# Performance work log

Measured on AMD Instinct MI355X. Metric: run time of the kernel, lower is better.

## Reference

```python
import jax, jax.numpy as jnp
import numpy as np

N_NODES = 50000
N_EDGES = 600000
N_FEAT = 128
N_DIMS = 128
N_CLSS = 10


def setup_inputs() -> dict:
    key = jax.random.key(0)
    ks = jax.random.split(key, 9)
    x = jax.random.normal(ks[0], (N_NODES, N_FEAT), dtype=jnp.float32)
    edge_index = jax.random.randint(ks[1], (2, N_EDGES), 0, N_NODES, dtype=jnp.int32)
    edge_weight = jax.random.uniform(ks[2], (N_EDGES,), dtype=jnp.float32)
    # Glorot-ish init for learned params
    W1 = jax.random.normal(ks[3], (N_FEAT, N_DIMS), dtype=jnp.float32) * (1.0 / np.sqrt(N_FEAT))
    b1 = jnp.zeros((N_DIMS,), dtype=jnp.float32)
    W2 = jax.random.normal(ks[4], (N_DIMS, N_DIMS), dtype=jnp.float32) * (1.0 / np.sqrt(N_DIMS))
    b2 = jnp.zeros((N_DIMS,), dtype=jnp.float32)
    Wc = jax.random.normal(ks[5], (N_DIMS, N_CLSS), dtype=jnp.float32) * (1.0 / np.sqrt(N_DIMS))
    bc = jnp.zeros((N_CLSS,), dtype=jnp.float32)
    return {"x": x, "edge_index": edge_index, "edge_weight": edge_weight,
            "W1": W1, "b1": b1, "W2": W2, "b2": b2, "Wc": Wc, "bc": bc}


def gcn_conv(x, W, b, src, dst, ew, n_nodes):
    """PyG GCNConv (add_self_loops=True, improved=False, bias=True).
    out[i] = sum_{(j->i) in E} d_i^-1/2 * w_ji * d_j^-1/2 * (xW)[j]
             + d_i^-1 * (xW)[i]  (self loop, weight 1) + b
    where d_i = 1 + sum of incoming edge weights at i.
    """
    h = x @ W                                                   # [N, D]
    deg = jax.ops.segment_sum(ew, dst, num_segments=n_nodes) + 1.0  # self-loop weight 1
    dinv = jax.lax.rsqrt(deg)                                   # deg >= 1, no inf
    norm = dinv[src] * ew * dinv[dst]                           # [E]
    agg = jax.ops.segment_sum(h[src] * norm[:, None], dst, num_segments=n_nodes)
    agg = agg + h * (dinv * dinv)[:, None]                      # self-loop term
    return agg + b


def reference(x, edge_index, edge_weight, W1, b1, W2, b2, Wc, bc):
    n = x.shape[0]
    src, dst = edge_index[0], edge_index[1]
    h = jax.nn.relu(gcn_conv(x, W1, b1, src, dst, edge_weight, n))
    # dropout is identity in eval mode
    h = gcn_conv(h, W2, b2, src, dst, edge_weight, n)
    h = jax.nn.relu(h)
    return h @ Wc + bc
```

## Files before the change

### kernel.cpp

```cpp
#include <hip/hip_runtime.h>
#include <hip/hip_bf16.h>

#define N_NODES 50000
#define N_EDGES 600000
#define NC 10

typedef __attribute__((ext_vector_type(8))) __bf16 bf16x8;
typedef __attribute__((ext_vector_type(4))) float f32x4;

__device__ __forceinline__ unsigned short f2bf(float f) {
    unsigned u = __float_as_uint(f);
    u += 0x7fff + ((u >> 16) & 1);
    return (unsigned short)(u >> 16);
}

__global__ void k_zero(int4* __restrict__ p, int n4) {
    int i = blockIdx.x * blockDim.x + threadIdx.x;
    if (i < n4) p[i] = make_int4(0, 0, 0, 0);
}

__global__ void k_x2b(const float4* __restrict__ in, ushort4* __restrict__ out, int n4) {
    int i = blockIdx.x * blockDim.x + threadIdx.x;
    if (i >= n4) return;
    float4 v = in[i];
    ushort4 o;
    o.x = f2bf(v.x); o.y = f2bf(v.y); o.z = f2bf(v.z); o.w = f2bf(v.w);
    out[i] = o;
}

__global__ void k_wt(const float* __restrict__ W, unsigned short* __restrict__ Wt) {
    int i = blockIdx.x * 256 + threadIdx.x;
    int n = i >> 7, k = i & 127;
    Wt[n * 128 + k] = f2bf(W[k * 128 + n]);
}

__global__ void k_count(const int4* __restrict__ dst4, int* __restrict__ cnt,
                        int4* __restrict__ ord4) {
    int i = blockIdx.x * blockDim.x + threadIdx.x;
    if (i >= N_EDGES / 4) return;
    int4 d = dst4[i];
    int4 o;
    o.x = atomicAdd(&cnt[d.x], 1);
    o.y = atomicAdd(&cnt[d.y], 1);
    o.z = atomicAdd(&cnt[d.z], 1);
    o.w = atomicAdd(&cnt[d.w], 1);
    ord4[i] = o;
}

__global__ void k_scan1(const int* __restrict__ cnt, int* __restrict__ rowptr,
                        int* __restrict__ bsum, int n) {
    __shared__ int sh[256];
    int t = threadIdx.x;
    int i = blockIdx.x * 256 + t;
    int v = (i < n) ? cnt[i] : 0;
    sh[t] = v;
    __syncthreads();
    for (int off = 1; off < 256; off <<= 1) {
        int x = 0;
        if (t >= off) x = sh[t - off];
        __syncthreads();
        sh[t] += x;
        __syncthreads();
    }
    if (i < n) rowptr[i] = sh[t] - v;
    if (t == 255) bsum[blockIdx.x] = sh[255];
}

__global__ void k_scan2(int* __restrict__ bsum, int nb) {
    __shared__ int sh[256];
    int t = threadIdx.x;
    int v = (t < nb) ? bsum[t] : 0;
    sh[t] = v;
    __syncthreads();
    for (int off = 1; off < 256; off <<= 1) {
        int x = 0;
        if (t >= off) x = sh[t - off];
        __syncthreads();
        sh[t] += x;
        __syncthreads();
    }
    if (t < nb) bsum[t] = sh[t] - v;
}

__global__ void k_scan3(int* __restrict__ rowptr, const int* __restrict__ bsum, int n) {
    int t = threadIdx.x;
    int i = blockIdx.x * 256 + t;
    if (i < n) rowptr[i] += bsum[blockIdx.x];
    if (blockIdx.x == 0 && t == 0) rowptr[n] = N_EDGES;
}

__global__ void k_scatter(const int* __restrict__ src, const int* __restrict__ dst,
                          const float* __restrict__ ew, const int* __restrict__ ord,
                          const int* __restrict__ rowptr,
                          int* __restrict__ esrc, float* __restrict__ ew2) {
    int e = blockIdx.x * blockDim.x + threadIdx.x;
    if (e >= N_EDGES) return;
    int pos = rowptr[dst[e]] + ord[e];
    esrc[pos] = src[e];
    ew2[pos]  = ew[e];
}

__global__ void k_deg(const int* __restrict__ rowptr, const float* __restrict__ ew2,
                      float* __restrict__ dinv) {
    int i = blockIdx.x * blockDim.x + threadIdx.x;
    if (i >= N_NODES) return;
    int p1 = rowptr[i + 1];
    float s = 1.0f;
    for (int p = rowptr[i]; p < p1; ++p) s += ew2[p];
    dinv[i] = rsqrtf(s);
}

__global__ void k_norm(const int* __restrict__ rowptr, const int* __restrict__ esrc,
                       const float* __restrict__ ew2, const float* __restrict__ dinv,
                       float* __restrict__ enorm) {
    int i = blockIdx.x * blockDim.x + threadIdx.x;
    if (i >= N_NODES) return;
    float di = dinv[i];
    int p  = rowptr[i];
    int p1 = rowptr[i + 1];
    for (; p + 4 <= p1; p += 4) {
        int s0 = esrc[p], s1 = esrc[p+1], s2 = esrc[p+2], s3 = esrc[p+3];
        float d0 = dinv[s0], d1 = dinv[s1], d2 = dinv[s2], d3 = dinv[s3];
        enorm[p]   = d0 * ew2[p]   * di;
        enorm[p+1] = d1 * ew2[p+1] * di;
        enorm[p+2] = d2 * ew2[p+2] * di;
        enorm[p+3] = d3 * ew2[p+3] * di;
    }
    for (; p < p1; ++p) enorm[p] = dinv[esrc[p]] * ew2[p] * di;
}

__global__ __launch_bounds__(256) void k_gemm_mfma(const unsigned short* __restrict__ Xb,
                                                   const unsigned short* __restrict__ Wt,
                                                   unsigned short* __restrict__ Yb, int M) {
    __shared__ unsigned short Al[64 * 128];
    __shared__ unsigned short Bl[128 * 128];
    int t = threadIdx.x;
    int row0 = blockIdx.x * 64;

    for (int i = t; i < 2048; i += 256) {
        int r = i >> 4, q = i & 15;
        *(bf16x8*)(Bl + r * 128 + ((q ^ (r & 7)) << 3)) =
            *(const bf16x8*)(Wt + r * 128 + (q << 3));
    }
    for (int i = t; i < 1024; i += 256) {
        int r = i >> 4, q = i & 15;
        int gr = row0 + r;
        bf16x8 v;
        if (gr < M) {
            v = *(const bf16x8*)(Xb + (size_t)gr * 128 + (q << 3));
        } else {
#pragma unroll
            for (int j = 0; j < 8; ++j) v[j] = (__bf16)0.0f;
        }
        *(bf16x8*)(Al + r * 128 + ((q ^ (r & 7)) << 3)) = v;
    }
    __syncthreads();

    int l  = t & 63;
    int w  = t >> 6;
    int ar = (w << 4) + (l & 15);
    int kq = l >> 4;

    bf16x8 af[4];
#pragma unroll
    for (int s = 0; s < 4; ++s) {
        int g = ((s << 2) + kq) ^ (l & 7);
        af[s] = *(const bf16x8*)(Al + ar * 128 + (g << 3));
    }

    f32x4 acc[8];
#pragma unroll
    for (int c = 0; c < 8; ++c)
#pragma unroll
        for (int j = 0; j < 4; ++j) acc[c][j] = 0.0f;

#pragma unroll
    for (int c = 0; c < 8; ++c) {
        int br = (c << 4) + (l & 15);
#pragma unroll
        for (int s = 0; s < 4; ++s) {
            int g = ((s << 2) + kq) ^ (l & 7);
            bf16x8 bf = *(const bf16x8*)(Bl + br * 128 + (g << 3));
            acc[c] = __builtin_amdgcn_mfma_f32_16x16x32_bf16(af[s], bf, acc[c], 0, 0, 0);
        }
    }

    int orow = row0 + (w << 4) + ((l >> 4) << 2);
    int ocol = l & 15;
#pragma unroll
    for (int c = 0; c < 8; ++c) {
#pragma unroll
        for (int j = 0; j < 4; ++j) {
            int r = orow + j;
            if (r < M) Yb[(size_t)r * 128 + (c << 4) + ocol] = f2bf(acc[c][j]);
        }
    }
}

template <int MODE>
__global__ __launch_bounds__(256) void k_agg(const unsigned* __restrict__ hb,
                                             const int* __restrict__ rowptr,
                                             const int* __restrict__ esrc,
                                             const float* __restrict__ enorm,
                                             const float* __restrict__ dinv,
                                             const float* __restrict__ bias,
                                             const float* __restrict__ Wc,
                                             const float* __restrict__ bc,
                                             float* __restrict__ out) {
    int wid  = (blockIdx.x * blockDim.x + threadIdx.x) >> 6;
    int lane = threadIdx.x & 63;
    if (wid >= N_NODES) return;
    wid = __builtin_amdgcn_readfirstlane(wid);
    int p  = __builtin_amdgcn_readfirstlane(rowptr[wid]);
    int p1 = __builtin_amdgcn_readfirstlane(rowptr[wid + 1]);
    float di  = dinv[wid];
    float di2 = di * di;
    unsigned sv = hb[(size_t)wid * 64 + lane];
    float2 acc;
    acc.x = __uint_as_float(sv << 16) * di2;
    acc.y = __uint_as_float(sv & 0xffff0000u) * di2;

    while (p + 12 <= p1) {
        int s[12]; float w[12]; unsigned v[12];
#pragma unroll
        for (int i = 0; i < 12; ++i) {
            s[i] = __builtin_amdgcn_readfirstlane(esrc[p + i]);
            w[i] = enorm[p + i];
        }
#pragma unroll
        for (int i = 0; i < 12; ++i) v[i] = hb[(size_t)s[i] * 64 + lane];
#pragma unroll
        for (int i = 0; i < 12; ++i) {
            acc.x += w[i] * __uint_as_float(v[i] << 16);
            acc.y += w[i] * __uint_as_float(v[i] & 0xffff0000u);
        }
        p += 12;
    }
    while (p + 4 <= p1) {
        int s[4]; float w[4]; unsigned v[4];
#pragma unroll
        for (int i = 0; i < 4; ++i) {
            s[i] = __builtin_amdgcn_readfirstlane(esrc[p + i]);
            w[i] = enorm[p + i];
        }
#pragma unroll
        for (int i = 0; i < 4; ++i) v[i] = hb[(size_t)s[i] * 64 + lane];
#pragma unroll
        for (int i = 0; i < 4; ++i) {
            acc.x += w[i] * __uint_as_float(v[i] << 16);
            acc.y += w[i] * __uint_as_float(v[i] & 0xffff0000u);
        }
        p += 4;
    }
    for (; p < p1; ++p) {
        int s = __builtin_amdgcn_readfirstlane(esrc[p]);
        float w = enorm[p];
        unsigned v = hb[(size_t)s * 64 + lane];
        acc.x += w * __uint_as_float(v << 16);
        acc.y += w * __uint_as_float(v & 0xffff0000u);
    }

    float2 bv = ((const float2*)bias)[lane];
    acc.x = fmaxf(acc.x + bv.x, 0.f);
    acc.y = fmaxf(acc.y + bv.y, 0.f);
    if (MODE == 0) {
        unsigned lo = f2bf(acc.x), hi = f2bf(acc.y);
        ((unsigned*)out)[(size_t)wid * 64 + lane] = lo | (hi << 16);
    } else {
        int k0 = 2 * lane;
        float r[NC];
#pragma unroll
        for (int c = 0; c < NC; ++c)
            r[c] = acc.x * Wc[k0 * NC + c] + acc.y * Wc[(k0 + 1) * NC + c];
#pragma unroll
        for (int off = 32; off; off >>= 1)
#pragma unroll
            for (int c = 0; c < NC; ++c)
                r[c] += __shfl_xor(r[c], off, 64);
        if (lane < NC) out[(size_t)wid * NC + lane] = r[lane] + bc[lane];
    }
}

extern "C" void kernel_launch(void* const* d_in, const int* in_sizes, int n_in,
                              void* d_out, int out_size, void* d_ws, size_t ws_size,
                              hipStream_t stream) {
    const float* x   = (const float*)d_in[0];
    const int*   ei  = (const int*)d_in[1];
    const float* ew  = (const float*)d_in[2];
    const float* W1  = (const float*)d_in[3];
    const float* b1  = (const float*)d_in[4];
    const float* W2  = (const float*)d_in[5];
    const float* b2  = (const float*)d_in[6];
    const float* Wc  = (const float*)d_in[7];
    const float* bc  = (const float*)d_in[8];
    float*       out = (float*)d_out;

    const int* src = ei;
    const int* dst = ei + N_EDGES;

    size_t off = 0;
    auto carve = [&](size_t bytes) {
        void* p = (char*)d_ws + off;
        off += (bytes + 255) & ~(size_t)255;
        return p;
    };
    unsigned short* xb  = (unsigned short*)carve((size_t)N_NODES * 128 * 2);
    unsigned short* hb  = (unsigned short*)carve((size_t)N_NODES * 128 * 2);
    unsigned short* hb1 = (unsigned short*)carve((size_t)N_NODES * 128 * 2);
    unsigned short* wt1 = (unsigned short*)carve(128 * 128 * 2);
    unsigned short* wt2 = (unsigned short*)carve(128 * 128 * 2);
    float* dinv   = (float*)carve((size_t)N_NODES * 4);
    int*   cnt    = (int*)carve((size_t)N_NODES * 4);
    int*   rowptr = (int*)carve((size_t)(N_NODES + 1) * 4);
    int*   bsum   = (int*)carve(256 * 4);
    int*   ord    = (int*)carve((size_t)N_EDGES * 4);
    int*   esrc   = (int*)carve((size_t)N_EDGES * 4);
    float* ew2    = (float*)carve((size_t)N_EDGES * 4);
    float* enorm  = (float*)carve((size_t)N_EDGES * 4);
    (void)ws_size; (void)n_in; (void)in_sizes; (void)out_size;

    int eb = (N_EDGES + 255) / 256;
    int nb = (N_NODES + 255) / 256;

    k_zero<<<(N_NODES / 4 + 255) / 256, 256, 0, stream>>>((int4*)cnt, N_NODES / 4);
    k_count<<<(N_EDGES / 4 + 255) / 256, 256, 0, stream>>>((const int4*)dst, cnt, (int4*)ord);
    k_scan1<<<nb, 256, 0, stream>>>(cnt, rowptr, bsum, N_NODES);
    k_scan2<<<1, 256, 0, stream>>>(bsum, nb);
    k_scan3<<<nb, 256, 0, stream>>>(rowptr, bsum, N_NODES);
    k_scatter<<<eb, 256, 0, stream>>>(src, dst, ew, ord, rowptr, esrc, ew2);
    k_deg<<<nb, 256, 0, stream>>>(rowptr, ew2, dinv);
    k_norm<<<nb, 256, 0, stream>>>(rowptr, esrc, ew2, dinv, enorm);

    int n4 = N_NODES * 128 / 4;
    k_x2b<<<(n4 + 255) / 256, 256, 0, stream>>>((const float4*)x, (ushort4*)xb, n4);
    k_wt<<<64, 256, 0, stream>>>(W1, wt1);
    k_wt<<<64, 256, 0, stream>>>(W2, wt2);

    int gb = (N_NODES + 63) / 64;
    k_gemm_mfma<<<gb, 256, 0, stream>>>(xb, wt1, hb, N_NODES);
    k_agg<0><<<(N_NODES + 3) / 4, 256, 0, stream>>>((const unsigned*)hb, rowptr, esrc,
                                                    enorm, dinv, b1, Wc, bc, (float*)hb1);
    k_gemm_mfma<<<gb, 256, 0, stream>>>(hb1, wt2, hb, N_NODES);
    k_agg<1><<<(N_NODES + 3) / 4, 256, 0, stream>>>((const unsigned*)hb, rowptr, esrc,
                                                    enorm, dinv, b2, Wc, bc, out);
}
```

Baseline: 172.4 us.

## Fuse fp32-to-bf16 conversion into first GEMM and merge prep kernels

Removes the separate x-to-bf16 pass: the first GEMM now loads fp32 x and converts while staging into LDS. Weight transposes are merged with edge counting, and the edge scatter is merged with the first GEMM, so independent work shares one launch. This cuts kernel launches and the intermediate bf16 copy of x. The aggregation loop is widened from 12 to 16 edges per batch, and edge weights are made wave-uniform via readfirstlane, at the cost of more registers.

Result: faster. 157.9 us (-8.4%).

```diff
diff --git a/kernel.cpp b/kernel.cpp
--- a/kernel.cpp
+++ b/kernel.cpp
@@ -4,8 +4,10 @@
 #define N_NODES 50000
 #define N_EDGES 600000
 #define NC 10
+#define GB ((N_NODES + 63) / 64)
 
 typedef __attribute__((ext_vector_type(8))) __bf16 bf16x8;
+typedef __attribute__((ext_vector_type(8))) unsigned short u16x8;
 typedef __attribute__((ext_vector_type(4))) float f32x4;
 
 __device__ __forceinline__ unsigned short f2bf(float f) {
@@ -13,38 +15,39 @@
     u += 0x7fff + ((u >> 16) & 1);
     return (unsigned short)(u >> 16);
 }
+__device__ __forceinline__ int rfl(int x) { return __builtin_amdgcn_readfirstlane(x); }
+__device__ __forceinline__ float rflf(float x) {
+    return __uint_as_float(__builtin_amdgcn_readfirstlane(__float_as_uint(x)));
+}
 
 __global__ void k_zero(int4* __restrict__ p, int n4) {
     int i = blockIdx.x * blockDim.x + threadIdx.x;
     if (i < n4) p[i] = make_int4(0, 0, 0, 0);
 }
 
-__global__ void k_x2b(const float4* __restrict__ in, ushort4* __restrict__ out, int n4) {
-    int i = blockIdx.x * blockDim.x + threadIdx.x;
-    if (i >= n4) return;
-    float4 v = in[i];
-    ushort4 o;
-    o.x = f2bf(v.x); o.y = f2bf(v.y); o.z = f2bf(v.z); o.w = f2bf(v.w);
-    out[i] = o;
-}
-
-__global__ void k_wt(const float* __restrict__ W, unsigned short* __restrict__ Wt) {
-    int i = blockIdx.x * 256 + threadIdx.x;
-    int n = i >> 7, k = i & 127;
-    Wt[n * 128 + k] = f2bf(W[k * 128 + n]);
-}
-
-__global__ void k_count(const int4* __restrict__ dst4, int* __restrict__ cnt,
-                        int4* __restrict__ ord4) {
-    int i = blockIdx.x * blockDim.x + threadIdx.x;
-    if (i >= N_EDGES / 4) return;
-    int4 d = dst4[i];
-    int4 o;
-    o.x = atomicAdd(&cnt[d.x], 1);
-    o.y = atomicAdd(&cnt[d.y], 1);
-    o.z = atomicAdd(&cnt[d.z], 1);
-    o.w = atomicAdd(&cnt[d.w], 1);
-    ord4[i] = o;
+__global__ void k_prep(const float* __restrict__ W1, const float* __restrict__ W2,
+                       unsigned short* __restrict__ wt1, unsigned short* __restrict__ wt2,
+                       const int4* __restrict__ dst4, int* __restrict__ cnt,
+                       int4* __restrict__ ord4) {
+    int b = blockIdx.x;
+    if (b < 128) {
+        const float* W = (b < 64) ? W1 : W2;
+        unsigned short* Wt = (b < 64) ? wt1 : wt2;
+        int i = (b & 63) * 256 + threadIdx.x;
+        int n = i >> 7, k = i & 127;
+        Wt[n * 128 + k] = f2bf(W[k * 128 + n]);
+    } else {
+        int i = (b - 128) * 256 + threadIdx.x;
+        if (i < N_EDGES / 4) {
+            int4 d = dst4[i];
+            int4 o;
+            o.x = atomicAdd(&cnt[d.x], 1);
+            o.y = atomicAdd(&cnt[d.y], 1);
+            o.z = atomicAdd(&cnt[d.z], 1);
+            o.w = atomicAdd(&cnt[d.w], 1);
+            ord4[i] = o;
+        }
+    }
 }
 
 __global__ void k_scan1(const int* __restrict__ cnt, int* __restrict__ rowptr,
@@ -89,15 +92,117 @@
     if (blockIdx.x == 0 && t == 0) rowptr[n] = N_EDGES;
 }
 
-__global__ void k_scatter(const int* __restrict__ src, const int* __restrict__ dst,
-                          const float* __restrict__ ew, const int* __restrict__ ord,
-                          const int* __restrict__ rowptr,
-                          int* __restrict__ esrc, float* __restrict__ ew2) {
-    int e = blockIdx.x * blockDim.x + threadIdx.x;
-    if (e >= N_EDGES) return;
-    int pos = rowptr[dst[e]] + ord[e];
-    esrc[pos] = src[e];
-    ew2[pos]  = ew[e];
+template <int FP32IN>
+__device__ __forceinline__ void gemm_body(unsigned short* Al, unsigned short* Bl,
+                                          const void* __restrict__ Xin,
+                                          const unsigned short* __restrict__ Wt,
+                                          unsigned short* __restrict__ Yb,
+                                          int M, int row0) {
+    int t = threadIdx.x;
+    for (int i = t; i < 2048; i += 256) {
+        int r = i >> 4, q = i & 15;
+        *(u16x8*)(Bl + r * 128 + ((q ^ (r & 7)) << 3)) =
+            *(const u16x8*)(Wt + r * 128 + (q << 3));
+    }
+    for (int i = t; i < 1024; i += 256) {
+        int r = i >> 4, q = i & 15;
+        int gr = row0 + r;
+        u16x8 v;
+        if (FP32IN) {
+            const float* X = (const float*)Xin;
+            if (gr < M) {
+                float4 f0 = *(const float4*)(X + (size_t)gr * 128 + (q << 3));
+                float4 f1 = *(const float4*)(X + (size_t)gr * 128 + (q << 3) + 4);
+                v[0] = f2bf(f0.x); v[1] = f2bf(f0.y); v[2] = f2bf(f0.z); v[3] = f2bf(f0.w);
+                v[4] = f2bf(f1.x); v[5] = f2bf(f1.y); v[6] = f2bf(f1.z); v[7] = f2bf(f1.w);
+            } else {
+#pragma unroll
+                for (int j = 0; j < 8; ++j) v[j] = 0;
+            }
+        } else {
+            const unsigned short* X = (const unsigned short*)Xin;
+            if (gr < M) {
+                v = *(const u16x8*)(X + (size_t)gr * 128 + (q << 3));
+            } else {
+#pragma unroll
+                for (int j = 0; j < 8; ++j) v[j] = 0;
+            }
+        }
+        *(u16x8*)(Al + r * 128 + ((q ^ (r & 7)) << 3)) = v;
+    }
+    __syncthreads();
+
+    int l  = t & 63;
+    int w  = t >> 6;
+    int ar = (w << 4) + (l & 15);
+    int kq = l >> 4;
+
+    bf16x8 af[4];
+#pragma unroll
+    for (int s = 0; s < 4; ++s) {
+        int g = ((s << 2) + kq) ^ (l & 7);
+        af[s] = *(const bf16x8*)(Al + ar * 128 + (g << 3));
+    }
+
+    f32x4 acc[8];
+#pragma unroll
+    for (int c = 0; c < 8; ++c)
+#pragma unroll
+        for (int j = 0; j < 4; ++j) acc[c][j] = 0.0f;
+
+#pragma unroll
+    for (int c = 0; c < 8; ++c) {
+        int br = (c << 4) + (l & 15);
+#pragma unroll
+        for (int s = 0; s < 4; ++s) {
+            int g = ((s << 2) + kq) ^ (l & 7);
+            bf16x8 bf = *(const bf16x8*)(Bl + br * 128 + (g << 3));
+            acc[c] = __builtin_amdgcn_mfma_f32_16x16x32_bf16(af[s], bf, acc[c], 0, 0, 0);
+        }
+    }
+
+    int orow = row0 + (w << 4) + ((l >> 4) << 2);
+    int ocol = l & 15;
+#pragma unroll
+    for (int c = 0; c < 8; ++c) {
+#pragma unroll
+        for (int j = 0; j < 4; ++j) {
+            int r = orow + j;
+            if (r < M) Yb[(size_t)r * 128 + (c << 4) + ocol] = f2bf(acc[c][j]);
+        }
+    }
+}
+
+__global__ __launch_bounds__(256) void k_sg(const float* __restrict__ X,
+                                            const unsigned short* __restrict__ Wt,
+                                            unsigned short* __restrict__ Yb, int M,
+                                            const int* __restrict__ src,
+                                            const int* __restrict__ dst,
+                                            const float* __restrict__ ew,
+                                            const int* __restrict__ ord,
+                                            const int* __restrict__ rowptr,
+                                            int* __restrict__ esrc,
+                                            float* __restrict__ ew2) {
+    __shared__ unsigned short Al[64 * 128];
+    __shared__ unsigned short Bl[128 * 128];
+    if (blockIdx.x < GB) {
+        gemm_body<1>(Al, Bl, X, Wt, Yb, M, blockIdx.x * 64);
+    } else {
+        int e = (blockIdx.x - GB) * 256 + threadIdx.x;
+        if (e < N_EDGES) {
+            int pos = rowptr[dst[e]] + ord[e];
+            esrc[pos] = src[e];
+            ew2[pos]  = ew[e];
+        }
+    }
+}
+
+__global__ __launch_bounds__(256) void k_gemm_mfma(const unsigned short* __restrict__ Xb,
+                                                   const unsigned short* __restrict__ Wt,
+                                                   unsigned short* __restrict__ Yb, int M) {
+    __shared__ unsigned short Al[64 * 128];
+    __shared__ unsigned short Bl[128 * 128];
+    gemm_body<0>(Al, Bl, Xb, Wt, Yb, M, blockIdx.x * 64);
 }
 
 __global__ void k_deg(const int* __restrict__ rowptr, const float* __restrict__ ew2,
@@ -129,74 +234,6 @@
     for (; p < p1; ++p) enorm[p] = dinv[esrc[p]] * ew2[p] * di;
 }
 
-__global__ __launch_bounds__(256) void k_gemm_mfma(const unsigned short* __restrict__ Xb,
-                                                   const unsigned short* __restrict__ Wt,
-                                                   unsigned short* __restrict__ Yb, int M) {
-    __shared__ unsigned short Al[64 * 128];
-    __shared__ unsigned short Bl[128 * 128];
-    int t = threadIdx.x;
-    int row0 = blockIdx.x * 64;
-
-    for (int i = t; i < 2048; i += 256) {
-        int r = i >> 4, q = i & 15;
-        *(bf16x8*)(Bl + r * 128 + ((q ^ (r & 7)) << 3)) =
-            *(const bf16x8*)(Wt + r * 128 + (q << 3));
-    }
-    for (int i = t; i < 1024; i += 256) {
-        int r = i >> 4, q = i & 15;
-        int gr = row0 + r;
-        bf16x8 v;
-        if (gr < M) {
-            v = *(const bf16x8*)(Xb + (size_t)gr * 128 + (q << 3));
-        } else {
-#pragma unroll
-            for (int j = 0; j < 8; ++j) v[j] = (__bf16)0.0f;
-        }
-        *(bf16x8*)(Al + r * 128 + ((q ^ (r & 7)) << 3)) = v;
-    }
-    __syncthreads();
-
-    int l  = t & 63;
-    int w  = t >> 6;
-    int ar = (w << 4) + (l & 15);
-    int kq = l >> 4;
-
-    bf16x8 af[4];
-#pragma unroll
-    for (int s = 0; s < 4; ++s) {
-        int g = ((s << 2) + kq) ^ (l & 7);
-        af[s] = *(const bf16x8*)(Al + ar * 128 + (g << 3));
-    }
-
-    f32x4 acc[8];
-#pragma unroll
-    for (int c = 0; c < 8; ++c)
-#pragma unroll
-        for (int j = 0; j < 4; ++j) acc[c][j] = 0.0f;
-
-#pragma unroll
-    for (int c = 0; c < 8; ++c) {
-        int br = (c << 4) + (l & 15);
-#pragma unroll
-        for (int s = 0; s < 4; ++s) {
-            int g = ((s << 2) + kq) ^ (l & 7);
-            bf16x8 bf = *(const bf16x8*)(Bl + br * 128 + (g << 3));
-            acc[c] = __builtin_amdgcn_mfma_f32_16x16x32_bf16(af[s], bf, acc[c], 0, 0, 0);
-        }
-    }
-
-    int orow = row0 + (w << 4) + ((l >> 4) << 2);
-    int ocol = l & 15;
-#pragma unroll
-    for (int c = 0; c < 8; ++c) {
-#pragma unroll
-        for (int j = 0; j < 4; ++j) {
-            int r = orow + j;
-            if (r < M) Yb[(size_t)r * 128 + (c << 4) + ocol] = f2bf(acc[c][j]);
-        }
-    }
-}
-
 template <int MODE>
 __global__ __launch_bounds__(256) void k_agg(const unsigned* __restrict__ hb,
                                              const int* __restrict__ rowptr,
@@ -210,9 +247,9 @@
     int wid  = (blockIdx.x * blockDim.x + threadIdx.x) >> 6;
     int lane = threadIdx.x & 63;
     if (wid >= N_NODES) return;
-    wid = __builtin_amdgcn_readfirstlane(wid);
-    int p  = __builtin_amdgcn_readfirstlane(rowptr[wid]);
-    int p1 = __builtin_amdgcn_readfirstlane(rowptr[wid + 1]);
+    wid = rfl(wid);
+    int p  = rfl(rowptr[wid]);
+    int p1 = rfl(rowptr[wid + 1]);
     float di  = dinv[wid];
     float di2 = di * di;
     unsigned sv = hb[(size_t)wid * 64 + lane];
@@ -220,28 +257,28 @@
     acc.x = __uint_as_float(sv << 16) * di2;
     acc.y = __uint_as_float(sv & 0xffff0000u) * di2;
 
-    while (p + 12 <= p1) {
-        int s[12]; float w[12]; unsigned v[12];
-#pragma unroll
-        for (int i = 0; i < 12; ++i) {
-            s[i] = __builtin_amdgcn_readfirstlane(esrc[p + i]);
-            w[i] = enorm[p + i];
-        }
-#pragma unroll
-        for (int i = 0; i < 12; ++i) v[i] = hb[(size_t)s[i] * 64 + lane];
-#pragma unroll
-        for (int i = 0; i < 12; ++i) {
+    while (p + 16 <= p1) {
+        int s[16]; float w[16]; unsigned v[16];
+#pragma unroll
+        for (int i = 0; i < 16; ++i) {
+            s[i] = rfl(esrc[p + i]);
+            w[i] = rflf(enorm[p + i]);
+        }
+#pragma unroll
+        for (int i = 0; i < 16; ++i) v[i] = hb[(size_t)s[i] * 64 + lane];
+#pragma unroll
+        for (int i = 0; i < 16; ++i) {
             acc.x += w[i] * __uint_as_float(v[i] << 16);
             acc.y += w[i] * __uint_as_float(v[i] & 0xffff0000u);
         }
-        p += 12;
+        p += 16;
     }
     while (p + 4 <= p1) {
         int s[4]; float w[4]; unsigned v[4];
 #pragma unroll
         for (int i = 0; i < 4; ++i) {
-            s[i] = __builtin_amdgcn_readfirstlane(esrc[p + i]);
-            w[i] = enorm[p + i];
+            s[i] = rfl(esrc[p + i]);
+            w[i] = rflf(enorm[p + i]);
         }
 #pragma unroll
         for (int i = 0; i < 4; ++i) v[i] = hb[(size_t)s[i] * 64 + lane];
@@ -253,8 +290,8 @@
         p += 4;
     }
     for (; p < p1; ++p) {
-        int s = __builtin_amdgcn_readfirstlane(esrc[p]);
-        float w = enorm[p];
+        int s = rfl(esrc[p]);
+        float w = rflf(enorm[p]);
         unsigned v = hb[(size_t)s * 64 + lane];
         acc.x += w * __uint_as_float(v << 16);
         acc.y += w * __uint_as_float(v & 0xffff0000u);
@@ -304,7 +341,6 @@
         off += (bytes + 255) & ~(size_t)255;
         return p;
     };
-    unsigned short* xb  = (unsigned short*)carve((size_t)N_NODES * 128 * 2);
     unsigned short* hb  = (unsigned short*)carve((size_t)N_NODES * 128 * 2);
     unsigned short* hb1 = (unsigned short*)carve((size_t)N_NODES * 128 * 2);
     unsigned short* wt1 = (unsigned short*)carve(128 * 128 * 2);
@@ -319,28 +355,23 @@
     float* enorm  = (float*)carve((size_t)N_EDGES * 4);
     (void)ws_size; (void)n_in; (void)in_sizes; (void)out_size;
 
+    int nb = (N_NODES + 255) / 256;
     int eb = (N_EDGES + 255) / 256;
-    int nb = (N_NODES + 255) / 256;
 
     k_zero<<<(N_NODES / 4 + 255) / 256, 256, 0, stream>>>((int4*)cnt, N_NODES / 4);
-    k_count<<<(N_EDGES / 4 + 255) / 256, 256, 0, stream>>>((const int4*)dst, cnt, (int4*)ord);
+    k_prep<<<128 + (N_EDGES / 4 + 255) / 256, 256, 0, stream>>>(
+        W1, W2, wt1, wt2, (const int4*)dst, cnt, (int4*)ord);
     k_scan1<<<nb, 256, 0, stream>>>(cnt, rowptr, bsum, N_NODES);
     k_scan2<<<1, 256, 0, stream>>>(bsum, nb);
     k_scan3<<<nb, 256, 0, stream>>>(rowptr, bsum, N_NODES);
-    k_scatter<<<eb, 256, 0, stream>>>(src, dst, ew, ord, rowptr, esrc, ew2);
+    k_sg<<<GB + eb, 256, 0, stream>>>(x, wt1, hb, N_NODES,
+                                      src, dst, ew, ord, rowptr, esrc, ew2);
     k_deg<<<nb, 256, 0, stream>>>(rowptr, ew2, dinv);
     k_norm<<<nb, 256, 0, stream>>>(rowptr, esrc, ew2, dinv, enorm);
 
-    int n4 = N_NODES * 128 / 4;
-    k_x2b<<<(n4 + 255) / 256, 256, 0, stream>>>((const float4*)x, (ushort4*)xb, n4);
-    k_wt<<<64, 256, 0, stream>>>(W1, wt1);
-    k_wt<<<64, 256, 0, stream>>>(W2, wt2);
-
-    int gb = (N_NODES + 63) / 64;
-    k_gemm_mfma<<<gb, 256, 0, stream>>>(xb, wt1, hb, N_NODES);
     k_agg<0><<<(N_NODES + 3) / 4, 256, 0, stream>>>((const unsigned*)hb, rowptr, esrc,
                                                     enorm, dinv, b1, Wc, bc, (float*)hb1);
-    k_gemm_mfma<<<gb, 256, 0, stream>>>(hb1, wt2, hb, N_NODES);
+    k_gemm_mfma<<<GB, 256, 0, stream>>>(hb1, wt2, hb, N_NODES);
     k_agg<1><<<(N_NODES + 3) / 4, 256, 0, stream>>>((const unsigned*)hb, rowptr, esrc,
                                                     enorm, dinv, b2, Wc, bc, out);
 }
```
